# Optimization experiments

Measured on AMD Instinct MI355X. Metric: run time of the kernel, lower is better.

## Reference

```python
import jax, jax.numpy as jnp
import numpy as np

# ---- module geometry ----
BULK = 64          # bulk (J2) integration points, 3 comps each
COH = 32           # cohesive integration points, 2 comps each
LS = BULK * 3 + COH * 2  # = 256, material layer width

# ---- J2 plasticity material constants (plane-stress, linear isotropic hardening) ----
E_MOD = 200.0
NU = 0.3
SY0 = 2.0
HARD = 10.0
G_MOD = E_MOD / (2.0 * (1.0 + NU))
_c = E_MOD / (1.0 - NU * NU)
C_EL = np.array([[_c, _c * NU, 0.0], [_c * NU, _c, 0.0], [0.0, 0.0, _c * (1.0 - NU) / 2.0]], dtype=np.float32)
C_INV = np.linalg.inv(C_EL).astype(np.float32)

# ---- Turon cohesive-zone constants (bilinear damage law) ----
K_PEN = 50.0       # penalty stiffness
DELTA0 = 0.1       # damage-onset effective jump
DELTAF = 1.0       # full-failure effective jump


def j2_update(eps, epsp, epbar):
    # eps, epsp: [B,P,3]; epbar: [B,P]. Radial-return with linear hardening.
    sig_tr = jnp.einsum('bpi,ji->bpj', eps - epsp, jnp.asarray(C_EL))
    s1, s2, s12 = sig_tr[..., 0], sig_tr[..., 1], sig_tr[..., 2]
    seq = jnp.sqrt(jnp.maximum(s1 * s1 - s1 * s2 + s2 * s2 + 3.0 * s12 * s12, 1e-12))
    f = seq - (SY0 + HARD * epbar)
    plastic = f > 0.0
    dep = jnp.where(plastic, f / (3.0 * G_MOD + HARD), 0.0)
    r = (SY0 + HARD * (epbar + dep)) / seq
    sig = jnp.where(plastic[..., None], r[..., None] * sig_tr, sig_tr)
    epsp_new = jnp.where(plastic[..., None], eps - jnp.einsum('bpj,ij->bpi', sig, jnp.asarray(C_INV)), epsp)
    return sig, epsp_new, epbar + dep


def coh_update(jump, hist):
    # jump: [B,P,2] (normal, shear); hist: [B,P] max effective jump (damage history).
    dn, ds = jump[..., 0], jump[..., 1]
    lam = jnp.sqrt(jnp.maximum(jnp.maximum(dn, 0.0) ** 2 + ds * ds, 1e-12))
    hist_new = jnp.maximum(hist, lam)
    dmg = jnp.clip(DELTAF * (hist_new - DELTA0) / (jnp.maximum(hist_new, 1e-12) * (DELTAF - DELTA0)), 0.0, 1.0)
    tn = K_PEN * dn * jnp.where(dn > 0.0, 1.0 - dmg, 1.0)  # compression is undamaged
    ts = (1.0 - dmg) * K_PEN * ds
    return jnp.stack([tn, ts], axis=-1), hist_new


def setup_inputs() -> dict:
    key = jax.random.key(0)
    k1, k2, k3 = jax.random.split(key, 3)
    x = jax.random.normal(k1, (256, 1024, 16), dtype=jnp.float32)
    W1 = jax.random.normal(k2, (LS, 16), dtype=jnp.float32) * 0.1
    W2 = jax.random.normal(k3, (16, LS), dtype=jnp.float32) * 0.1
    return {"x": x, "W1": W1, "W2": W2}


def reference(x, W1, W2):
    B, T, F = x.shape
    # fc1 applied to every (batch, time) slice (original loops; here one GEMM)
    h = jnp.einsum('btf,lf->btl', x, W1)  # [B,T,LS]
    h_t = jnp.transpose(h, (1, 0, 2))     # [T,B,LS] for the time scan

    epsp0 = jnp.zeros((B, BULK, 3), dtype=x.dtype)
    epbar0 = jnp.zeros((B, BULK), dtype=x.dtype)
    hist0 = jnp.zeros((B, COH), dtype=x.dtype)

    def step(carry, ht):
        epsp, epbar, hist = carry
        eps = ht[:, : BULK * 3].reshape(B, BULK, 3)
        jmp = ht[:, BULK * 3:].reshape(B, COH, 2)
        sig, epsp, epbar = j2_update(eps, epsp, epbar)   # update + commit per step
        trac, hist = coh_update(jmp, hist)
        y = jnp.concatenate([sig.reshape(B, -1), trac.reshape(B, -1)], axis=-1)
        return (epsp, epbar, hist), y

    _, ys = jax.lax.scan(step, (epsp0, epbar0, hist0), h_t)  # [T,B,LS]
    ys = jnp.transpose(ys, (1, 0, 2))  # [B,T,LS]
    # softLayer fc2: linear with softplus-constrained (non-negative) weights
    out = jnp.einsum('btl,ol->bto', ys, jax.nn.softplus(W2))
    return out
```

## Files before the change

kernel.cpp:

```cpp
#include <hip/hip_runtime.h>
#include <cmath>
#include <cstdint>

#define BATCH  256
#define TT     1024
#define FIN    16
#define NBULK  64
#define NCOH   32
#define TC     32
#define NCHUNK (TT / TC)
#define SROW   328
#define YSS    336

typedef __attribute__((ext_vector_type(8))) short short8;
typedef __attribute__((ext_vector_type(4))) float floatx4;

__device__ __forceinline__ unsigned short f2bf_rne(float f) {
    union { float f; unsigned int i; } v; v.f = f;
    unsigned int b = v.i;
    return (unsigned short)((b + 0x7FFFu + ((b >> 16) & 1u)) >> 16);
}
__device__ __forceinline__ float u2f(unsigned int u) {
    union { unsigned int i; float f; } v; v.i = u; return v.f;
}

#define BARRIER() asm volatile("s_waitcnt lgkmcnt(0)\n\ts_barrier" ::: "memory")

#define MC00   219.78021978021977f
#define MC01   65.93406593406593f
#define MC22   76.92307692307692f
#define MSY0   2.0f
#define AK     0.958466453674121406f
#define BK     0.041533546325878594f

__global__ __launch_bounds__(256, 1)
void fused_mat_kernel(const float* __restrict__ x,
                      const float* __restrict__ w1,
                      const float* __restrict__ w2,
                      float* __restrict__ out)
{
    __shared__ __attribute__((aligned(16))) float          s_h[2][TC][SROW];
    __shared__ __attribute__((aligned(16))) unsigned short s_y[2][TC][YSS];

    const int tid  = threadIdx.x;
    const int b    = blockIdx.x;
    const int lane = tid & 63;
    const int wv   = tid >> 6;
    const int m    = lane & 15;
    const int q    = lane >> 4;

    const size_t xrow = (size_t)b * TT;

    short8 w1p[16];
    short8 w1c[4];
    short8 vf[10];
    uint4  rxc[2][2], rxp[2][2];

    auto emit = [&](const short8* axv, const short8* adxv, float* dst) {
        #pragma unroll
        for (int mt = 0; mt < 2; ++mt) {
            float* drow = dst + (mt * 16 + m) * SROW + q * 4;
            #pragma unroll
            for (int n = 0; n < 20; ++n) {
                floatx4 acc = {0.f, 0.f, 0.f, 0.f};
                acc = (n < 16)
                    ? __builtin_amdgcn_mfma_f32_16x16x32_bf16(w1p[n], adxv[mt], acc, 0, 0, 0)
                    : __builtin_amdgcn_mfma_f32_16x16x32_bf16(w1c[n - 16], axv[mt], acc, 0, 0, 0);
                *(floatx4*)(drow + n * 16) = acc;
            }
        }
    };

    if (wv == 2) {
        #pragma unroll
        for (int n = 0; n < 16; ++n) {
            #pragma unroll
            for (int j = 0; j < 8; ++j) {
                float v = 0.f;
                if (q < 2) {
                    const int lp = n * 16 + m, c = lp >> 2, cm = lp & 3, f = q * 8 + j;
                    if (cm < 3) {
                        const float wa  = w1[(3 * c + 0) * FIN + f];
                        const float wb  = w1[(3 * c + 1) * FIN + f];
                        const float wcc = w1[(3 * c + 2) * FIN + f];
                        v = (cm == 0) ? fmaf(MC01, wb, MC00 * wa)
                          : (cm == 1) ? fmaf(MC00, wb, MC01 * wa)
                                      : MC22 * wcc;
                    }
                }
                w1p[n][j] = (short)f2bf_rne(v);
            }
        }
        #pragma unroll
        for (int n = 0; n < 4; ++n) {
            #pragma unroll
            for (int j = 0; j < 8; ++j) {
                unsigned short v = 0;
                if (q < 2) v = f2bf_rne(w1[(192 + n * 16 + m) * FIN + q * 8 + j]);
                w1c[n][j] = (short)v;
            }
        }
        short8 ax0[2], adx0[2];
        #pragma unroll
        for (int mt = 0; mt < 2; ++mt) {
            #pragma unroll
            for (int j = 0; j < 8; ++j) {
                float xc = 0.f, xp = 0.f;
                if (q < 2) {
                    const int rowB = mt * 16 + m;
                    xc = x[(xrow + rowB) * FIN + q * 8 + j];
                    if (rowB > 0) xp = x[(xrow + rowB - 1) * FIN + q * 8 + j];
                }
                ax0[mt][j]  = (short)f2bf_rne(xc);
                adx0[mt][j] = (short)f2bf_rne(xc - xp);
            }
        }
        if (q < 2) {
            #pragma unroll
            for (int mt = 0; mt < 2; ++mt) {
                const int rowB = TC + mt * 16 + m;
                const float* xc = x + (xrow + rowB) * FIN + q * 8;
                const float* xp = x + (xrow + rowB - 1) * FIN + q * 8;
                rxc[mt][0] = *(const uint4*)xc;  rxc[mt][1] = *(const uint4*)(xc + 4);
                rxp[mt][0] = *(const uint4*)xp;  rxp[mt][1] = *(const uint4*)(xp + 4);
            }
        }
        emit(ax0, adx0, &s_h[0][0][0]);
    } else if (wv == 3) {
        #pragma unroll
        for (int ks = 0; ks < 10; ++ks) {
            #pragma unroll
            for (int j = 0; j < 8; ++j) {
                const int p = ks * 32 + q * 8 + j;
                unsigned short v = 0;
                if (p < 256) {
                    const int comp = p & 3;
                    if (comp < 3) {
                        const int l = 3 * (p >> 2) + comp;
                        float xv = w2[m * 256 + l];
                        float sp = fmaxf(xv, 0.0f) + log1pf(expf(-fabsf(xv)));
                        v = f2bf_rne(sp);
                    }
                } else {
                    const int l = p - 64;
                    float xv = w2[m * 256 + l];
                    float sp = fmaxf(xv, 0.0f) + log1pf(expf(-fabsf(xv)));
                    v = f2bf_rne(sp);
                }
                vf[ks][j] = (short)v;
            }
        }
    }

    float sg0 = 0.f, sg1 = 0.f, sg2 = 0.f, syv = MSY0, pre = AK * MSY0;
    float hist = 0.f;

    __syncthreads();

    for (int i = 0; i <= NCHUNK; ++i) {
        if (wv == 0) {
            if (i < NCHUNK) {
                const float* hb = &s_h[i & 1][0][0] + 4 * lane;
                unsigned short* yb = &s_y[i & 1][0][0] + 4 * lane;
                floatx4 dbuf[4];
                #pragma unroll
                for (int p = 0; p < 4; ++p) dbuf[p] = *(const floatx4*)(hb + p * SROW);
                auto stepb = [&](floatx4 dv, int t) {
                    const float t0 = sg0 + dv.x, t1 = sg1 + dv.y, t2 = sg2 + dv.z;
                    const float s01 = t0 - t1;
                    const float u   = t2 * t2;
                    const float w3  = fmaf(u, 2.0f, u);
                    const float bb  = fmaf(t1, t1, w3);
                    const float qq  = fmaxf(fmaf(t0, s01, bb), 1e-12f);
                    const float rs  = __builtin_amdgcn_rsqf(qq);
                    const float seq = qq * rs;
                    const float rr  = fminf(fmaf(pre, rs, BK), 1.0f);
                    sg0 = rr * t0; sg1 = rr * t1; sg2 = rr * t2;
                    syv = fmaxf(syv, fmaf(BK, seq, pre));
                    pre = AK * syv;
                    unsigned int r0, r1;
                    asm("v_cvt_pk_bf16_f32 %0, %1, %2" : "=v"(r0) : "v"(sg0), "v"(sg1));
                    asm("v_cvt_pk_bf16_f32 %0, %1, %2" : "=v"(r1) : "v"(sg2), "v"(sg2));
                    uint2 pk; pk.x = r0; pk.y = r1;
                    *(uint2*)(yb + t * YSS) = pk;
                };
                #pragma unroll 4
                for (int t = 0; t < TC - 4; ++t) {
                    const floatx4 dv = dbuf[t & 3];
                    dbuf[t & 3] = *(const floatx4*)(hb + (t + 4) * SROW);
                    stepb(dv, t);
                }
                #pragma unroll
                for (int t = TC - 4; t < TC; ++t) stepb(dbuf[t & 3], t);
            }
        } else if (wv == 1) {
            if (i < NCHUNK && lane < NCOH) {
                const float* hc = &s_h[i & 1][0][0] + 256 + 2 * lane;
                unsigned short* yc = &s_y[i & 1][0][0] + 256 + 2 * lane;
                float2 jbuf[4];
                #pragma unroll
                for (int p = 0; p < 4; ++p) jbuf[p] = *(const float2*)(hc + p * SROW);
                auto stepc = [&](float2 jv, int t) {
                    const float dn = jv.x, ds = jv.y;
                    const float dnp = fmaxf(dn, 0.0f);
                    const float lam = __builtin_amdgcn_sqrtf(fmaxf(fmaf(dnp, dnp, ds * ds), 1e-12f));
                    hist = fmaxf(hist, lam);
                    float dmg = (hist - 0.1f) * __builtin_amdgcn_rcpf(hist * 0.9f);
                    dmg = fminf(fmaxf(dmg, 0.0f), 1.0f);
                    const float om = 1.0f - dmg;
                    const float tn = 50.0f * dn * (dn > 0.0f ? om : 1.0f);
                    const float ts = om * 50.0f * ds;
                    unsigned int r;
                    asm("v_cvt_pk_bf16_f32 %0, %1, %2" : "=v"(r) : "v"(tn), "v"(ts));
                    *(unsigned int*)(yc + t * YSS) = r;
                };
                #pragma unroll 4
                for (int t = 0; t < TC - 4; ++t) {
                    const float2 jv = jbuf[t & 3];
                    jbuf[t & 3] = *(const float2*)(hc + (t + 4) * SROW);
                    stepc(jv, t);
                }
                #pragma unroll
                for (int t = TC - 4; t < TC; ++t) stepc(jbuf[t & 3], t);
            }
        } else if (wv == 2) {
            if (i + 1 < NCHUNK) {
                short8 ax[2], adx[2];
                #pragma unroll
                for (int mt = 0; mt < 2; ++mt) {
                    const unsigned int wc[8] = {rxc[mt][0].x, rxc[mt][0].y, rxc[mt][0].z, rxc[mt][0].w,
                                                rxc[mt][1].x, rxc[mt][1].y, rxc[mt][1].z, rxc[mt][1].w};
                    const unsigned int wp[8] = {rxp[mt][0].x, rxp[mt][0].y, rxp[mt][0].z, rxp[mt][0].w,
                                                rxp[mt][1].x, rxp[mt][1].y, rxp[mt][1].z, rxp[mt][1].w};
                    #pragma unroll
                    for (int j = 0; j < 8; ++j) {
                        unsigned short va = 0, vd = 0;
                        if (q < 2) {
                            const float xc = u2f(wc[j]), xp = u2f(wp[j]);
                            va = f2bf_rne(xc);
                            vd = f2bf_rne(xc - xp);
                        }
                        ax[mt][j]  = (short)va;
                        adx[mt][j] = (short)vd;
                    }
                }
                if (i + 2 < NCHUNK && q < 2) {
                    #pragma unroll
                    for (int mt = 0; mt < 2; ++mt) {
                        const int rowB = (i + 2) * TC + mt * 16 + m;
                        const float* xc = x + (xrow + rowB) * FIN + q * 8;
                        const float* xp = x + (xrow + rowB - 1) * FIN + q * 8;
                        rxc[mt][0] = *(const uint4*)xc;  rxc[mt][1] = *(const uint4*)(xc + 4);
                        rxp[mt][0] = *(const uint4*)xp;  rxp[mt][1] = *(const uint4*)(xp + 4);
                    }
                }
                emit(ax, adx, &s_h[(i + 1) & 1][0][0]);
            }
        } else {
            if (i >= 1) {
                const int tb = (i - 1) * TC;
                const unsigned short* yb = &s_y[(i - 1) & 1][0][0];
                #pragma unroll
                for (int mt = 0; mt < 2; ++mt) {
                    floatx4 a0 = {0.f, 0.f, 0.f, 0.f};
                    floatx4 a1 = {0.f, 0.f, 0.f, 0.f};
                    #pragma unroll
                    for (int ks = 0; ks < 5; ++ks) {
                        const short8* yp = (const short8*)(yb + (mt * 16 + m) * YSS + ks * 32 + q * 8);
                        a0 = __builtin_amdgcn_mfma_f32_16x16x32_bf16(*yp, vf[ks], a0, 0, 0, 0);
                    }
                    #pragma unroll
                    for (int ks = 5; ks < 10; ++ks) {
                        const short8* yp = (const short8*)(yb + (mt * 16 + m) * YSS + ks * 32 + q * 8);
                        a1 = __builtin_amdgcn_mfma_f32_16x16x32_bf16(*yp, vf[ks], a1, 0, 0, 0);
                    }
                    #pragma unroll
                    for (int r = 0; r < 4; ++r)
                        out[(xrow + tb + mt * 16 + q * 4 + r) * FIN + m] = a0[r] + a1[r];
                }
            }
        }
        BARRIER();
    }
}

extern "C" void kernel_launch(void* const* d_in, const int* in_sizes, int n_in,
                              void* d_out, int out_size, void* d_ws, size_t ws_size,
                              hipStream_t stream) {
    const float* x  = (const float*)d_in[0];
    const float* w1 = (const float*)d_in[1];
    const float* w2 = (const float*)d_in[2];
    float* out = (float*)d_out;
    fused_mat_kernel<<<BATCH, 256, 0, stream>>>(x, w1, w2, out);
}
```

Baseline: 167.8 us.

## Widen block to 8 waves and split scan, GEMM1 and GEMM2 roles across them

Doubles the workgroup to 512 threads. The bulk J2 scan is split across two half-populated waves, the fc1 MFMA work is split across three waves (two delta-x groups and one cohesive group), and the fc2 output GEMM uses one wave per M-tile. Per-chunk scan inputs are also preloaded fully into registers instead of using a 4-deep rolling buffer. The goal is to shorten the critical path of each chunk stage before the barrier. The cost is more register pressure from the 32-element preload and lower lane utilisation in the scan waves.

```diff
diff --git a/kernel.cpp b/kernel.cpp
--- a/kernel.cpp
+++ b/kernel.cpp
@@ -5,8 +5,6 @@
 #define BATCH  256
 #define TT     1024
 #define FIN    16
-#define NBULK  64
-#define NCOH   32
 #define TC     32
 #define NCHUNK (TT / TC)
 #define SROW   328
@@ -33,7 +31,8 @@
 #define AK     0.958466453674121406f
 #define BK     0.041533546325878594f
 
-__global__ __launch_bounds__(256, 1)
+
+__global__ __launch_bounds__(512, 1)
 void fused_mat_kernel(const float* __restrict__ x,
                       const float* __restrict__ w1,
                       const float* __restrict__ w2,
@@ -51,68 +50,77 @@
 
     const size_t xrow = (size_t)b * TT;
 
-    short8 w1p[16];
-    short8 w1c[4];
+    const bool isG     = (wv == 3) | (wv == 4) | (wv == 7);
+    const int  hw      = (wv == 3) ? 0 : (wv == 4) ? 1 : 2;
+    const int  nbase   = hw * 8;
+    const int  nfrag   = (hw == 2) ? 4 : 8;
+    const bool useDelta = (hw < 2);
+
+    short8 wfrag[8];
     short8 vf[10];
     uint4  rxc[2][2], rxp[2][2];
 
-    auto emit = [&](const short8* axv, const short8* adxv, float* dst) {
+    auto emit = [&](const short8* af, float* dst) {
         #pragma unroll
         for (int mt = 0; mt < 2; ++mt) {
-            float* drow = dst + (mt * 16 + m) * SROW + q * 4;
-            #pragma unroll
-            for (int n = 0; n < 20; ++n) {
-                floatx4 acc = {0.f, 0.f, 0.f, 0.f};
-                acc = (n < 16)
-                    ? __builtin_amdgcn_mfma_f32_16x16x32_bf16(w1p[n], adxv[mt], acc, 0, 0, 0)
-                    : __builtin_amdgcn_mfma_f32_16x16x32_bf16(w1c[n - 16], axv[mt], acc, 0, 0, 0);
-                *(floatx4*)(drow + n * 16) = acc;
+            float* drow = dst + (mt * 16 + m) * SROW + q * 4 + nbase * 16;
+            #pragma unroll
+            for (int j = 0; j < 8; ++j) {
+                if (j < nfrag) {
+                    floatx4 acc = {0.f, 0.f, 0.f, 0.f};
+                    acc = __builtin_amdgcn_mfma_f32_16x16x32_bf16(wfrag[j], af[mt], acc, 0, 0, 0);
+                    *(floatx4*)(drow + j * 16) = acc;
+                }
             }
         }
     };
 
-    if (wv == 2) {
-        #pragma unroll
-        for (int n = 0; n < 16; ++n) {
+    if (isG) {
+        #pragma unroll
+        for (int j = 0; j < 8; ++j) {
+            short8 fr;
+            #pragma unroll
+            for (int jj = 0; jj < 8; ++jj) fr[jj] = 0;
+            if (j < nfrag) {
+                const int n = nbase + j;
+                #pragma unroll
+                for (int jj = 0; jj < 8; ++jj) {
+                    float v = 0.f;
+                    if (q < 2) {
+                        const int f = q * 8 + jj;
+                        if (n < 16) {
+                            const int lp = n * 16 + m, c = lp >> 2, cm = lp & 3;
+                            if (cm < 3) {
+                                const float wa  = w1[(3 * c + 0) * FIN + f];
+                                const float wb  = w1[(3 * c + 1) * FIN + f];
+                                const float wcc = w1[(3 * c + 2) * FIN + f];
+                                v = (cm == 0) ? fmaf(MC01, wb, MC00 * wa)
+                                  : (cm == 1) ? fmaf(MC00, wb, MC01 * wa)
+                                              : MC22 * wcc;
+                            }
+                        } else {
+                            v = w1[(192 + (n - 16) * 16 + m) * FIN + f];
+                        }
+                    }
+                    fr[jj] = (short)f2bf_rne(v);
+                }
+            }
+            wfrag[j] = fr;
+        }
+        short8 af0[2];
+        #pragma unroll
+        for (int mt = 0; mt < 2; ++mt) {
             #pragma unroll
             for (int j = 0; j < 8; ++j) {
-                float v = 0.f;
-                if (q < 2) {
-                    const int lp = n * 16 + m, c = lp >> 2, cm = lp & 3, f = q * 8 + j;
-                    if (cm < 3) {
-                        const float wa  = w1[(3 * c + 0) * FIN + f];
-                        const float wb  = w1[(3 * c + 1) * FIN + f];
-                        const float wcc = w1[(3 * c + 2) * FIN + f];
-                        v = (cm == 0) ? fmaf(MC01, wb, MC00 * wa)
-                          : (cm == 1) ? fmaf(MC00, wb, MC01 * wa)
-                                      : MC22 * wcc;
-                    }
-                }
-                w1p[n][j] = (short)f2bf_rne(v);
-            }
-        }
-        #pragma unroll
-        for (int n = 0; n < 4; ++n) {
-            #pragma unroll
-            for (int j = 0; j < 8; ++j) {
-                unsigned short v = 0;
-                if (q < 2) v = f2bf_rne(w1[(192 + n * 16 + m) * FIN + q * 8 + j]);
-                w1c[n][j] = (short)v;
-            }
-        }
-        short8 ax0[2], adx0[2];
-        #pragma unroll
-        for (int mt = 0; mt < 2; ++mt) {
-            #pragma unroll
-            for (int j = 0; j < 8; ++j) {
-                float xc = 0.f, xp = 0.f;
+                float val = 0.f;
                 if (q < 2) {
                     const int rowB = mt * 16 + m;
-                    xc = x[(xrow + rowB) * FIN + q * 8 + j];
+                    const float xc = x[(xrow + rowB) * FIN + q * 8 + j];
+                    float xp = 0.f;
                     if (rowB > 0) xp = x[(xrow + rowB - 1) * FIN + q * 8 + j];
-                }
-                ax0[mt][j]  = (short)f2bf_rne(xc);
-                adx0[mt][j] = (short)f2bf_rne(xc - xp);
+                    val = useDelta ? (xc - xp) : xc;
+                }
+                af0[mt][j] = (short)f2bf_rne(val);
             }
         }
         if (q < 2) {
@@ -125,8 +133,8 @@
                 rxp[mt][0] = *(const uint4*)xp;  rxp[mt][1] = *(const uint4*)(xp + 4);
             }
         }
-        emit(ax0, adx0, &s_h[0][0][0]);
-    } else if (wv == 3) {
+        emit(af0, &s_h[0][0][0]);
+    } else if (wv == 5 || wv == 6) {
         #pragma unroll
         for (int ks = 0; ks < 10; ++ks) {
             #pragma unroll
@@ -158,14 +166,17 @@
     __syncthreads();
 
     for (int i = 0; i <= NCHUNK; ++i) {
-        if (wv == 0) {
-            if (i < NCHUNK) {
-                const float* hb = &s_h[i & 1][0][0] + 4 * lane;
-                unsigned short* yb = &s_y[i & 1][0][0] + 4 * lane;
-                floatx4 dbuf[4];
-                #pragma unroll
-                for (int p = 0; p < 4; ++p) dbuf[p] = *(const floatx4*)(hb + p * SROW);
-                auto stepb = [&](floatx4 dv, int t) {
+        if (wv < 2) {
+            if (i < NCHUNK && lane < 32) {
+                const int p = wv * 32 + lane;
+                const float* hb = &s_h[i & 1][0][0] + 4 * p;
+                unsigned short* yb = &s_y[i & 1][0][0] + 4 * p;
+                floatx4 dvv[TC];
+                #pragma unroll
+                for (int t = 0; t < TC; ++t) dvv[t] = *(const floatx4*)(hb + t * SROW);
+                #pragma unroll
+                for (int t = 0; t < TC; ++t) {
+                    const floatx4 dv = dvv[t];
                     const float t0 = sg0 + dv.x, t1 = sg1 + dv.y, t2 = sg2 + dv.z;
                     const float s01 = t0 - t1;
                     const float u   = t2 * t2;
@@ -183,25 +194,18 @@
                     asm("v_cvt_pk_bf16_f32 %0, %1, %2" : "=v"(r1) : "v"(sg2), "v"(sg2));
                     uint2 pk; pk.x = r0; pk.y = r1;
                     *(uint2*)(yb + t * YSS) = pk;
-                };
-                #pragma unroll 4
-                for (int t = 0; t < TC - 4; ++t) {
-                    const floatx4 dv = dbuf[t & 3];
-                    dbuf[t & 3] = *(const floatx4*)(hb + (t + 4) * SROW);
-                    stepb(dv, t);
-                }
-                #pragma unroll
-                for (int t = TC - 4; t < TC; ++t) stepb(dbuf[t & 3], t);
-            }
-        } else if (wv == 1) {
-            if (i < NCHUNK && lane < NCOH) {
+                }
+            }
+        } else if (wv == 2) {
+            if (i < NCHUNK && lane < 32) {
                 const float* hc = &s_h[i & 1][0][0] + 256 + 2 * lane;
                 unsigned short* yc = &s_y[i & 1][0][0] + 256 + 2 * lane;
-                float2 jbuf[4];
-                #pragma unroll
-                for (int p = 0; p < 4; ++p) jbuf[p] = *(const float2*)(hc + p * SROW);
-                auto stepc = [&](float2 jv, int t) {
-                    const float dn = jv.x, ds = jv.y;
+                float2 jvv[TC];
+                #pragma unroll
+                for (int t = 0; t < TC; ++t) jvv[t] = *(const float2*)(hc + t * SROW);
+                #pragma unroll
+                for (int t = 0; t < TC; ++t) {
+                    const float dn = jvv[t].x, ds = jvv[t].y;
                     const float dnp = fmaxf(dn, 0.0f);
                     const float lam = __builtin_amdgcn_sqrtf(fmaxf(fmaf(dnp, dnp, ds * ds), 1e-12f));
                     hist = fmaxf(hist, lam);
@@ -213,19 +217,11 @@
                     unsigned int r;
                     asm("v_cvt_pk_bf16_f32 %0, %1, %2" : "=v"(r) : "v"(tn), "v"(ts));
                     *(unsigned int*)(yc + t * YSS) = r;
-                };
-                #pragma unroll 4
-                for (int t = 0; t < TC - 4; ++t) {
-                    const float2 jv = jbuf[t & 3];
-                    jbuf[t & 3] = *(const float2*)(hc + (t + 4) * SROW);
-                    stepc(jv, t);
-                }
-                #pragma unroll
-                for (int t = TC - 4; t < TC; ++t) stepc(jbuf[t & 3], t);
-            }
-        } else if (wv == 2) {
+                }
+            }
+        } else if (isG) {
             if (i + 1 < NCHUNK) {
-                short8 ax[2], adx[2];
+                short8 af[2];
                 #pragma unroll
                 for (int mt = 0; mt < 2; ++mt) {
                     const unsigned int wc[8] = {rxc[mt][0].x, rxc[mt][0].y, rxc[mt][0].z, rxc[mt][0].w,
@@ -234,14 +230,13 @@
                                                 rxp[mt][1].x, rxp[mt][1].y, rxp[mt][1].z, rxp[mt][1].w};
                     #pragma unroll
                     for (int j = 0; j < 8; ++j) {
-                        unsigned short va = 0, vd = 0;
+                        unsigned short v = 0;
                         if (q < 2) {
                             const float xc = u2f(wc[j]), xp = u2f(wp[j]);
-                            va = f2bf_rne(xc);
-                            vd = f2bf_rne(xc - xp);
+                            const float val = useDelta ? (xc - xp) : xc;
+                            v = f2bf_rne(val);
                         }
-                        ax[mt][j]  = (short)va;
-                        adx[mt][j] = (short)vd;
+                        af[mt][j] = (short)v;
                     }
                 }
                 if (i + 2 < NCHUNK && q < 2) {
@@ -254,30 +249,28 @@
                         rxp[mt][0] = *(const uint4*)xp;  rxp[mt][1] = *(const uint4*)(xp + 4);
                     }
                 }
-                emit(ax, adx, &s_h[(i + 1) & 1][0][0]);
+                emit(af, &s_h[(i + 1) & 1][0][0]);
             }
         } else {
             if (i >= 1) {
+                const int mt = wv - 5;
                 const int tb = (i - 1) * TC;
                 const unsigned short* yb = &s_y[(i - 1) & 1][0][0];
-                #pragma unroll
-                for (int mt = 0; mt < 2; ++mt) {
-                    floatx4 a0 = {0.f, 0.f, 0.f, 0.f};
-                    floatx4 a1 = {0.f, 0.f, 0.f, 0.f};
-                    #pragma unroll
-                    for (int ks = 0; ks < 5; ++ks) {
-                        const short8* yp = (const short8*)(yb + (mt * 16 + m) * YSS + ks * 32 + q * 8);
-                        a0 = __builtin_amdgcn_mfma_f32_16x16x32_bf16(*yp, vf[ks], a0, 0, 0, 0);
-                    }
-                    #pragma unroll
-                    for (int ks = 5; ks < 10; ++ks) {
-                        const short8* yp = (const short8*)(yb + (mt * 16 + m) * YSS + ks * 32 + q * 8);
-                        a1 = __builtin_amdgcn_mfma_f32_16x16x32_bf16(*yp, vf[ks], a1, 0, 0, 0);
-                    }
-                    #pragma unroll
-                    for (int r = 0; r < 4; ++r)
-                        out[(xrow + tb + mt * 16 + q * 4 + r) * FIN + m] = a0[r] + a1[r];
-                }
+                floatx4 a0 = {0.f, 0.f, 0.f, 0.f};
+                floatx4 a1 = {0.f, 0.f, 0.f, 0.f};
+                #pragma unroll
+                for (int ks = 0; ks < 5; ++ks) {
+                    const short8* yp = (const short8*)(yb + (mt * 16 + m) * YSS + ks * 32 + q * 8);
+                    a0 = __builtin_amdgcn_mfma_f32_16x16x32_bf16(*yp, vf[ks], a0, 0, 0, 0);
+                }
+                #pragma unroll
+                for (int ks = 5; ks < 10; ++ks) {
+                    const short8* yp = (const short8*)(yb + (mt * 16 + m) * YSS + ks * 32 + q * 8);
+                    a1 = __builtin_amdgcn_mfma_f32_16x16x32_bf16(*yp, vf[ks], a1, 0, 0, 0);
+                }
+                #pragma unroll
+                for (int r = 0; r < 4; ++r)
+                    out[(xrow + tb + mt * 16 + q * 4 + r) * FIN + m] = a0[r] + a1[r];
             }
         }
         BARRIER();
@@ -291,5 +284,5 @@
     const float* w1 = (const float*)d_in[1];
     const float* w2 = (const float*)d_in[2];
     float* out = (float*)d_out;
-    fused_mat_kernel<<<BATCH, 256, 0, stream>>>(x, w1, w2, out);
-}
+    fused_mat_kernel<<<BATCH, 512, 0, stream>>>(x, w1, w2, out);
+}
```

New measurement: 145.3 us. -13.4%, faster.
